# Kernel optimization log

Measured on AMD Instinct MI355X. Metric: run time of the kernel, lower is better.

Reference implementation:

```python
import jax, jax.numpy as jnp
import numpy as np

# ---- constants matching init_kwargs ----
ALPHA = 1.0
SCALING = 12.0
RESP_INDEX = (0, 1, 2, 3)
N_TARGETS = len(RESP_INDEX)
NDAYS = 250  # number of distinct date ids; with N=2M and 250 ids all are present
N = 2_000_000
N_RESP = 5


def setup_inputs() -> dict:
    key = jax.random.key(0)
    k1, k2, k3, k4 = jax.random.split(key, 4)
    inputs = jax.random.normal(k1, (N, N_RESP), dtype=jnp.float32)
    targets = jax.random.normal(k2, (N, N_RESP), dtype=jnp.float32)
    weights = jax.random.uniform(k3, (N,), dtype=jnp.float32)
    date = jax.random.randint(k4, (N,), 0, NDAYS, dtype=jnp.int64)
    return {"inputs": inputs, "targets": targets, "weights": weights, "date": date}


def reference(inputs, targets, weights, date):
    # slice resp columns (resp_index is not None and len < 5)
    idx = jnp.asarray(RESP_INDEX)
    x = jax.nn.sigmoid(SCALING * inputs[..., idx])   # [N, 4]
    t = targets[..., idx]                            # [N, 4]

    # faithful to torch: inputs/targets flattened sample-major, while
    # weights/date are repeat-tiled (resp-major) -- same pairing as original.
    x = x.reshape(-1)                 # [4N], sample-major
    t = t.reshape(-1)                 # [4N], sample-major
    w = jnp.tile(weights, N_TARGETS)  # [4N], tiled
    d = jnp.tile(date, N_TARGETS)     # [4N], tiled

    # per-day grouped sum -> single-pass segment reduction
    Pi = jax.ops.segment_sum(w * t * x, d, num_segments=NDAYS)  # [NDAYS]

    sumPi = Pi.sum()
    # normalize == 'mean'
    loss = -ALPHA * sumPi * jnp.maximum(sumPi, 0.0) / jnp.sum(Pi * Pi) / NDAYS
    return loss
```

## Files before the change

### kernel.cpp

```cpp
#include <hip/hip_runtime.h>

#define NDAYS 250
#define SCALING 12.0f
#define NBLK 512
#define TPB 256
#define MIDB 64
#define RPM (NBLK / MIDB)

typedef float f4 __attribute__((ext_vector_type(4)));
typedef int   i4 __attribute__((ext_vector_type(4)));

__global__ __launch_bounds__(TPB) void pi_kernel(
    const float* __restrict__ inputs, const float* __restrict__ targets,
    const float* __restrict__ weights, const int* __restrict__ date,
    float* __restrict__ part, int n) {
    __shared__ float sPi[NDAYS];
    for (int i = threadIdx.x; i < NDAYS; i += TPB) sPi[i] = 0.0f;
    __syncthreads();

    const int nq = n >> 2;
    const int ns = n >> 4;
    const int s = blockIdx.x * TPB + threadIdx.x;
    if (s < ns) {
        float acc[16];
        #pragma unroll
        for (int mm = 0; mm < 16; ++mm) acc[mm] = 0.0f;

        #pragma unroll
        for (int q = 0; q < 4; ++q) {
            const size_t rowbase = ((size_t)q * nq + 4 * (size_t)s) * 5;
            const float* ip = inputs + rowbase;
            const float* tp = targets + rowbase;
            f4 in5[5], tg5[5];
            #pragma unroll
            for (int e = 0; e < 5; ++e) {
                in5[e] = *(const f4*)(ip + 4 * e);
                tg5[e] = *(const f4*)(tp + 4 * e);
            }
            const float* in_f = (const float*)in5;
            const float* tg_f = (const float*)tg5;
            #pragma unroll
            for (int r = 0; r < 4; ++r) {
                #pragma unroll
                for (int j = 0; j < 4; ++j) {
                    const float xin = in_f[5 * r + j];
                    const float e1 = __expf(-SCALING * xin);
                    const float sg = __builtin_amdgcn_rcpf(1.0f + e1);
                    acc[4 * r + j] += tg_f[5 * r + j] * sg;
                }
            }
        }

        const long m0 = (long)s << 4;
        f4 w4[4]; i4 d4[4];
        #pragma unroll
        for (int e = 0; e < 4; ++e) {
            w4[e] = *(const f4*)(weights + m0 + 4 * e);
            d4[e] = *(const i4*)(date + m0 + 4 * e);
        }
        const float* w_f = (const float*)w4;
        const int*   d_i = (const int*)d4;
        #pragma unroll
        for (int mm = 0; mm < 16; ++mm)
            atomicAdd(&sPi[d_i[mm]], acc[mm] * w_f[mm]);
    }

    __syncthreads();
    float* row = part + (size_t)blockIdx.x * NDAYS;
    for (int i = threadIdx.x; i < NDAYS; i += TPB) row[i] = sPi[i];
}

__global__ __launch_bounds__(TPB) void mid_kernel(const float* __restrict__ part,
                                                  float* __restrict__ part2) {
    const int c = threadIdx.x;
    if (c < NDAYS) {
        const float* p = part + (size_t)blockIdx.x * RPM * NDAYS + c;
        float a = 0.0f;
        #pragma unroll
        for (int r = 0; r < RPM; ++r) a += p[(size_t)r * NDAYS];
        part2[(size_t)blockIdx.x * NDAYS + c] = a;
    }
}

__global__ __launch_bounds__(TPB) void fin_kernel(const float* __restrict__ part2,
                                                  float* __restrict__ out) {
    __shared__ float ws_s[4], ws_q[4];
    const int t = threadIdx.x;
    float s = 0.0f, q = 0.0f;
    if (t < NDAYS) {
        float pc = 0.0f;
        #pragma unroll 8
        for (int r = 0; r < MIDB; ++r) pc += part2[(size_t)r * NDAYS + t];
        s = pc;
        q = pc * pc;
    }
    #pragma unroll
    for (int off = 32; off > 0; off >>= 1) {
        s += __shfl_down(s, off);
        q += __shfl_down(q, off);
    }
    if ((t & 63) == 0) {
        ws_s[t >> 6] = s;
        ws_q[t >> 6] = q;
    }
    __syncthreads();
    if (t == 0) {
        const float sumPi  = ws_s[0] + ws_s[1] + ws_s[2] + ws_s[3];
        const float sumPi2 = ws_q[0] + ws_q[1] + ws_q[2] + ws_q[3];
        out[0] = -1.0f * sumPi * fmaxf(sumPi, 0.0f) / sumPi2 / (float)NDAYS;
    }
}

extern "C" void kernel_launch(void* const* d_in, const int* in_sizes, int n_in,
                              void* d_out, int out_size, void* d_ws, size_t ws_size,
                              hipStream_t stream) {
    const float* inputs  = (const float*)d_in[0];
    const float* targets = (const float*)d_in[1];
    const float* weights = (const float*)d_in[2];
    const int*   date    = (const int*)d_in[3];
    float* out   = (float*)d_out;
    float* part  = (float*)d_ws;
    float* part2 = part + (size_t)NBLK * NDAYS;

    const int n = in_sizes[2];

    pi_kernel<<<NBLK, TPB, 0, stream>>>(inputs, targets, weights, date, part, n);
    mid_kernel<<<MIDB, TPB, 0, stream>>>(part, part2);
    fin_kernel<<<1, TPB, 0, stream>>>(part2, out);
}
```

Baseline: 131.3 us.

## Coalesce input/target loads by mapping threads to contiguous float4 chunks

Each block now handles a tile of 1024 rows and threads read consecutive float4 chunks of the row-major [N,5] arrays, instead of each thread reading 20 contiguous floats. This gives fully coalesced wavefront loads. Each float is mapped back to its sample and column with a multiply-shift divide by 5. Weights and dates are gathered per element with scalar loads, and the 5th column is masked out. In exchange it adds index arithmetic, scalar gathers, and 20 LDS atomics per thread, some of them dummy adds of zero spread over the lanes.

```diff
diff --git a/kernel.cpp b/kernel.cpp
--- a/kernel.cpp
+++ b/kernel.cpp
@@ -2,13 +2,13 @@
 
 #define NDAYS 250
 #define SCALING 12.0f
+#define TPB 256
 #define NBLK 512
-#define TPB 256
+#define TILE 1024
 #define MIDB 64
 #define RPM (NBLK / MIDB)
 
 typedef float f4 __attribute__((ext_vector_type(4)));
-typedef int   i4 __attribute__((ext_vector_type(4)));
 
 __global__ __launch_bounds__(TPB) void pi_kernel(
     const float* __restrict__ inputs, const float* __restrict__ targets,
@@ -19,50 +19,57 @@
     __syncthreads();
 
     const int nq = n >> 2;
-    const int ns = n >> 4;
-    const int s = blockIdx.x * TPB + threadIdx.x;
-    if (s < ns) {
-        float acc[16];
+    const int ii0 = blockIdx.x * TILE;
+    if (ii0 < nq) {
+        const int ts  = min(TILE, nq - ii0);
+        const int nfl = ts * 5;
+        const int lane = threadIdx.x & 63;
+
+        int   dy[5][4];
+        float wt[5][4];
         #pragma unroll
-        for (int mm = 0; mm < 16; ++mm) acc[mm] = 0.0f;
+        for (int e = 0; e < 5; ++e) {
+            const int c   = TPB * e + threadIdx.x;
+            const int fl0 = 4 * c;
+            #pragma unroll
+            for (int dlt = 0; dlt < 4; ++dlt) {
+                const int fl = fl0 + dlt;
+                const int si = (int)(((unsigned)fl * 52429u) >> 18);
+                const int j  = fl - 5 * si;
+                const bool valid = (fl < nfl) && (j < 4);
+                const int  m = valid ? (4 * (ii0 + si) + j) : 0;
+                wt[e][dlt] = valid ? weights[m] : 0.0f;
+                dy[e][dlt] = valid ? date[m] : lane;
+            }
+        }
 
+        float acc[5][4] = {};
         #pragma unroll
         for (int q = 0; q < 4; ++q) {
-            const size_t rowbase = ((size_t)q * nq + 4 * (size_t)s) * 5;
-            const float* ip = inputs + rowbase;
-            const float* tp = targets + rowbase;
-            f4 in5[5], tg5[5];
+            const size_t base = ((size_t)q * nq + ii0) * 5;
             #pragma unroll
             for (int e = 0; e < 5; ++e) {
-                in5[e] = *(const f4*)(ip + 4 * e);
-                tg5[e] = *(const f4*)(tp + 4 * e);
-            }
-            const float* in_f = (const float*)in5;
-            const float* tg_f = (const float*)tg5;
-            #pragma unroll
-            for (int r = 0; r < 4; ++r) {
+                const int c = TPB * e + threadIdx.x;
+                f4 inv = {0.0f, 0.0f, 0.0f, 0.0f};
+                f4 tgv = {0.0f, 0.0f, 0.0f, 0.0f};
+                if (4 * c < nfl) {
+                    inv = *(const f4*)(inputs + base + 4 * c);
+                    tgv = *(const f4*)(targets + base + 4 * c);
+                }
                 #pragma unroll
-                for (int j = 0; j < 4; ++j) {
-                    const float xin = in_f[5 * r + j];
-                    const float e1 = __expf(-SCALING * xin);
+                for (int dlt = 0; dlt < 4; ++dlt) {
+                    const float e1 = __expf(-SCALING * inv[dlt]);
                     const float sg = __builtin_amdgcn_rcpf(1.0f + e1);
-                    acc[4 * r + j] += tg_f[5 * r + j] * sg;
+                    acc[e][dlt] += tgv[dlt] * sg;
                 }
             }
         }
 
-        const long m0 = (long)s << 4;
-        f4 w4[4]; i4 d4[4];
         #pragma unroll
-        for (int e = 0; e < 4; ++e) {
-            w4[e] = *(const f4*)(weights + m0 + 4 * e);
-            d4[e] = *(const i4*)(date + m0 + 4 * e);
-        }
-        const float* w_f = (const float*)w4;
-        const int*   d_i = (const int*)d4;
-        #pragma unroll
-        for (int mm = 0; mm < 16; ++mm)
-            atomicAdd(&sPi[d_i[mm]], acc[mm] * w_f[mm]);
+        for (int e = 0; e < 5; ++e)
+            #pragma unroll
+            for (int dlt = 0; dlt < 4; ++dlt)
+                atomicAdd(&sPi[dy[e][dlt]], acc[e][dlt] * wt[e][dlt]);
     }
 
     __syncthreads();
```

Result: faster. 125.8 us (median of 2 runs) (-4.2%).
